# Kernel optimization log

Measured on AMD Instinct MI355X. Metric: run time of the kernel, lower is better.

Reference implementation:

```python
import jax, jax.numpy as jnp
import numpy as np

DIM = 384
HEADS = 6
DIM_HEAD = 64
INNER = HEADS * DIM_HEAD  # 384


def setup_inputs() -> dict:
    key = jax.random.key(0)
    ks = jax.random.split(key, 6)
    s = 0.02
    return {
        "x_q": jax.random.normal(ks[0], (8, 4096, DIM), dtype=jnp.float32),
        "x_kv": jax.random.normal(ks[1], (8, 4096, DIM), dtype=jnp.float32),
        "Wq": jax.random.normal(ks[2], (DIM, INNER), dtype=jnp.float32) * s,
        "Wkv": jax.random.normal(ks[3], (DIM, 2 * INNER), dtype=jnp.float32) * s,
        "Wout": jax.random.normal(ks[4], (INNER, DIM), dtype=jnp.float32) * s,
        "bout": jax.random.normal(ks[5], (DIM,), dtype=jnp.float32) * s,
    }


def _split_heads(t, b, n):
    # [b, n, h*d] -> [b, h, n, d]
    return t.reshape(b, n, HEADS, DIM_HEAD).transpose(0, 2, 1, 3)


def reference(x_q, x_kv, Wq, Wkv, Wout, bout):
    b, nq, _ = x_q.shape
    nkv = x_kv.shape[1]
    q = x_q @ Wq                      # [b, nq, inner]
    kv_proj = x_kv @ Wkv              # [b, nkv, 2*inner]
    k, v = jnp.split(kv_proj, 2, axis=-1)
    q = _split_heads(q, b, nq)        # [b, h, nq, d]
    k = _split_heads(k, b, nkv)       # [b, h, nkv, d]
    v = _split_heads(v, b, nkv)       # [b, h, nkv, d]
    q = jax.nn.elu(q) + 1.0
    k = jax.nn.elu(k) + 1.0
    kv = jnp.einsum('bhnd,bhnm->bhdm', k, v)             # [b, h, d, d]
    z = 1.0 / (jnp.einsum('bhnd,bhd->bhn', q, k.sum(axis=2)) + 1e-6)
    out = jnp.einsum('bhnd,bhdm->bhnm', q, kv) * z[..., None]  # [b, h, nq, d]
    out = out.transpose(0, 2, 1, 3).reshape(b, nq, INNER)
    return out @ Wout + bout
```

## Files before the change

kernel.cpp:

```cpp
#include <hip/hip_runtime.h>
#include <math.h>

#define BATCH 8
#define SEQ 4096
#define DIMSZ 384
#define HEADS 6
#define DH 64
#define MTOT (BATCH * SEQ)
#define KD 384

typedef short short8 __attribute__((ext_vector_type(8)));
typedef float floatx4 __attribute__((ext_vector_type(4)));
typedef unsigned short ushort4v __attribute__((ext_vector_type(4)));
typedef unsigned short ushort8v __attribute__((ext_vector_type(8)));
typedef unsigned int uint2v __attribute__((ext_vector_type(2)));
typedef unsigned int uint4v __attribute__((ext_vector_type(4)));

__device__ __forceinline__ float elu1(float x) { return x > 0.f ? x + 1.f : __expf(x); }

__device__ __forceinline__ unsigned short f2b(float f) {
    unsigned int u = __float_as_uint(f);
    u = (u + 0x7fffu + ((u >> 16) & 1u)) >> 16;
    return (unsigned short)u;
}
__device__ __forceinline__ float b2f(unsigned short u) {
    return __uint_as_float(((unsigned int)u) << 16);
}
__device__ __forceinline__ unsigned int f2b2(float lo, float hi) {
    unsigned int r;
    asm("v_cvt_pk_bf16_f32 %0, %1, %2" : "=v"(r) : "v"(lo), "v"(hi));
    return r;
}

__device__ __forceinline__ void gl16(const void* g, void* l) {
    __builtin_amdgcn_global_load_lds((const __attribute__((address_space(1))) unsigned int*)g,
                                     (__attribute__((address_space(3))) unsigned int*)l, 16, 0, 0);
}

#define BARRIER_EXEMPT8()                                              \
    do {                                                               \
        asm volatile("s_waitcnt vmcnt(8) lgkmcnt(0)" ::: "memory");    \
        __builtin_amdgcn_s_barrier();                                  \
        __builtin_amdgcn_sched_barrier(0);                             \
    } while (0)
#define BARRIER_EXEMPT4()                                              \
    do {                                                               \
        asm volatile("s_waitcnt vmcnt(4) lgkmcnt(0)" ::: "memory");    \
        __builtin_amdgcn_s_barrier();                                  \
        __builtin_amdgcn_sched_barrier(0);                             \
    } while (0)
#define BARRIER_DRAIN()                                                \
    do {                                                               \
        asm volatile("s_waitcnt vmcnt(0) lgkmcnt(0)" ::: "memory");    \
        __builtin_amdgcn_s_barrier();                                  \
        __builtin_amdgcn_sched_barrier(0);                             \
    } while (0)

__global__ __launch_bounds__(256) void conv_wt3(const float* __restrict__ Wq,
                                                const float* __restrict__ Wkv,
                                                const float* __restrict__ Wout,
                                                unsigned short* __restrict__ WqT,
                                                unsigned short* __restrict__ WkvT,
                                                unsigned short* __restrict__ WoutT) {
    __shared__ float tile[32][33];
    int bx = blockIdx.x;
    const float* W;
    unsigned short* WT;
    int N;
    if (bx < 12) { W = Wq; WT = WqT; N = DIMSZ; }
    else if (bx < 36) { W = Wkv; WT = WkvT; N = 2 * DIMSZ; bx -= 12; }
    else { W = Wout; WT = WoutT; N = DIMSZ; bx -= 36; }
    const int n0 = bx * 32, k0 = blockIdx.y * 32;
    const int tx = threadIdx.x & 31, ty = threadIdx.x >> 5;
#pragma unroll
    for (int i = 0; i < 32; i += 8) tile[ty + i][tx] = W[(size_t)(k0 + ty + i) * N + n0 + tx];
    __syncthreads();
#pragma unroll
    for (int i = 0; i < 32; i += 8)
        WT[(size_t)(n0 + ty + i) * KD + k0 + tx] = f2b(tile[tx][ty + i]);
}

__global__ __launch_bounds__(256, 3) void gemm_kv(const float* __restrict__ A,
                                                  const unsigned short* __restrict__ WkvT,
                                                  float* __restrict__ pkv,
                                                  float* __restrict__ pks) {
    __shared__ __align__(16) unsigned short buf[17408];
    __shared__ float ksLDS[128];
    unsigned short* As = buf;
    unsigned short* Bs = buf + 8192;
    const int tid = threadIdx.x;
    const int lane = tid & 63, wave = tid >> 6;
    const int l15 = lane & 15, qd = lane >> 4;
    const int fid = blockIdx.x;
    const int xcd = fid & 7;
    const int s = fid >> 3;
    const int h = s % HEADS;
    const int rtl = s / HEADS;
    const int row0 = (xcd * 32 + rtl) * 128;
    const int pidx = (xcd * HEADS + h) * 32 + rtl;
    const int wm = (wave & 1) * 64, wn = (wave >> 1) * 64;

    const float* Ab = A + (size_t)row0 * KD;
    const unsigned short* Bb = WkvT + (size_t)(h * DH) * KD;
    const int srow = tid >> 3;
    const int scol = (((tid & 7) ^ (srow & 7)) * 8);

    floatx4 zero = {0.f, 0.f, 0.f, 0.f};
    floatx4 acc[4][4];
#pragma unroll
    for (int i = 0; i < 4; ++i)
#pragma unroll
        for (int j = 0; j < 4; ++j) acc[i][j] = zero;

    const int sw = l15 & 7;
    float4 g0[4], g1[4];
#pragma unroll
    for (int i = 0; i < 4; ++i) {
        const float* src = Ab + (size_t)(i * 32 + srow) * KD + scol;
        g0[i] = *(const float4*)src;
        g1[i] = *(const float4*)(src + 4);
    }
#pragma unroll
    for (int kk = 0; kk < KD; kk += 64) {
        __syncthreads();
#pragma unroll
        for (int i = 0; i < 4; ++i)
            gl16(Bb + (size_t)(i * 32 + srow + (i >= 2 ? 320 : 0)) * KD + kk + scol,
                 Bs + i * 2048 + wave * 512);
#pragma unroll
        for (int i = 0; i < 4; ++i) {
            uint4v u;
            u[0] = f2b2(g0[i].x, g0[i].y);
            u[1] = f2b2(g0[i].z, g0[i].w);
            u[2] = f2b2(g1[i].x, g1[i].y);
            u[3] = f2b2(g1[i].z, g1[i].w);
            *(uint4v*)&As[i * 2048 + tid * 8] = u;
        }
        if (kk + 64 < KD) {
#pragma unroll
            for (int i = 0; i < 4; ++i) {
                const float* src = Ab + (size_t)(i * 32 + srow) * KD + kk + 64 + scol;
                g0[i] = *(const float4*)src;
                g1[i] = *(const float4*)(src + 4);
            }
            BARRIER_EXEMPT8();
        } else {
            BARRIER_DRAIN();
        }
#pragma unroll
        for (int t = 0; t < 2; ++t) {
            const int chnk = ((t * 4 + qd) ^ sw) * 8;
            short8 af[4], bfr[4];
#pragma unroll
            for (int mi = 0; mi < 4; ++mi)
                af[mi] = *(const short8*)&As[(wm + mi * 16 + l15) * 64 + chnk];
#pragma unroll
            for (int ni = 0; ni < 4; ++ni)
                bfr[ni] = *(const short8*)&Bs[(wn + ni * 16 + l15) * 64 + chnk];
#pragma unroll
            for (int mi = 0; mi < 4; ++mi)
#pragma unroll
                for (int ni = 0; ni < 4; ++ni)
                    acc[mi][ni] = __builtin_amdgcn_mfma_f32_16x16x32_bf16(af[mi], bfr[ni],
                                                                          acc[mi][ni], 0, 0, 0);
        }
    }

    __syncthreads();
    const bool kw = (wn == 0);
    float ksp[4] = {};
#pragma unroll
    for (int mi = 0; mi < 4; ++mi)
#pragma unroll
        for (int ni = 0; ni < 4; ++ni) {
            const int rb = wm + mi * 16 + qd * 4;
            const int cl = wn + ni * 16 + l15;
            float v0 = acc[mi][ni][0], v1 = acc[mi][ni][1];
            float v2 = acc[mi][ni][2], v3 = acc[mi][ni][3];
            if (kw) {
                v0 = elu1(v0); v1 = elu1(v1); v2 = elu1(v2); v3 = elu1(v3);
                ksp[ni] += (v0 + v1) + (v2 + v3);
            }
            uint2v o;
            o[0] = f2b2(v0, v1);
            o[1] = f2b2(v2, v3);
            *(uint2v*)&buf[cl * 136 + rb] = o;
        }
    if (kw) {
#pragma unroll
        for (int ni = 0; ni < 4; ++ni) {
            float v = ksp[ni];
            v += __shfl_xor(v, 16);
            v += __shfl_xor(v, 32);
            if (lane < 16) ksLDS[wave * 64 + ni * 16 + lane] = v;
        }
    }
    __syncthreads();
    floatx4 kva[4];
#pragma unroll
    for (int j = 0; j < 4; ++j) kva[j] = zero;
#pragma unroll
    for (int nk = 0; nk < 4; ++nk) {
        short8 afk = *(const short8*)&buf[(wave * 16 + l15) * 136 + nk * 32 + qd * 8];
#pragma unroll
        for (int nj = 0; nj < 4; ++nj) {
            short8 bfv = *(const short8*)&buf[(64 + nj * 16 + l15) * 136 + nk * 32 + qd * 8];
            kva[nj] = __builtin_amdgcn_mfma_f32_16x16x32_bf16(afk, bfv, kva[nj], 0, 0, 0);
        }
    }
    float* P = pkv + (size_t)pidx * 4096;
#pragma unroll
    for (int nj = 0; nj < 4; ++nj)
#pragma unroll
        for (int r = 0; r < 4; ++r)
            P[(wave * 16 + qd * 4 + r) * 64 + nj * 16 + l15] = kva[nj][r];
    if (tid < 64) pks[pidx * 64 + tid] = ksLDS[tid] + ksLDS[64 + tid];
}

__global__ __launch_bounds__(256) void kv_reduce(const float* __restrict__ pkv,
                                                 const float* __restrict__ pks,
                                                 unsigned short* __restrict__ kv_bf,
                                                 float* __restrict__ ksum_g) {
    const int bh = blockIdx.x >> 2, dc = blockIdx.x & 3;
    const int tid = threadIdx.x;
    unsigned short* kb = kv_bf + (size_t)bh * 4096;
    const int i0 = dc * 1024 + tid * 4;
    float4 sum = {0.f, 0.f, 0.f, 0.f};
#pragma unroll
    for (int c = 0; c < 32; ++c) {
        float4 p = *(const float4*)&pkv[(size_t)(bh * 32 + c) * 4096 + i0];
        sum.x += p.x; sum.y += p.y; sum.z += p.z; sum.w += p.w;
    }
    const int d = i0 >> 6, m = i0 & 63;
    kb[(m + 0) * 64 + d] = f2b(sum.x);
    kb[(m + 1) * 64 + d] = f2b(sum.y);
    kb[(m + 2) * 64 + d] = f2b(sum.z);
    kb[(m + 3) * 64 + d] = f2b(sum.w);
    if (dc == 0 && tid < 64) {
        float s = 0.f;
#pragma unroll
        for (int c = 0; c < 32; ++c) s += pks[(bh * 32 + c) * 64 + tid];
        ksum_g[bh * 64 + tid] = s;
    }
}

__global__ __launch_bounds__(256, 3) void gemm_q_attn(const float* __restrict__ A,
                                                      const unsigned short* __restrict__ WqT,
                                                      const unsigned short* __restrict__ kv_bf,
                                                      const float* __restrict__ ksum_g,
                                                      unsigned short* __restrict__ attn) {
    __shared__ __align__(16) unsigned short buf[17408];
    __shared__ float ksh[128];
    __shared__ float zsh[256];
    unsigned short* As = buf;
    unsigned short* Bs = buf + 8192;
    const int tid = threadIdx.x;
    const int lane = tid & 63, wave = tid >> 6;
    const int l15 = lane & 15, qd = lane >> 4;
    const int fid = blockIdx.x;
    const int xcd = fid & 7;
    const int s = fid >> 3;
    const int ct = s % 3;
    const int rtl = s / 3;
    const int row0 = (xcd * 32 + rtl) * 128;
    const int col0 = ct * 128;
    const int bh0 = xcd * HEADS + ct * 2;
    const int wd = (wave & 1) * 64, wn2 = (wave >> 1) * 64;

    if (tid < 128) ksh[tid] = ksum_g[bh0 * 64 + tid];

    const float* Ab = A + (size_t)row0 * KD;
    const unsigned short* Bb = WqT + (size_t)col0 * KD;
    const int srow = tid >> 3;
    const int scol = (((tid & 7) ^ (srow & 7)) * 8);

    floatx4 zero = {0.f, 0.f, 0.f, 0.f};
    floatx4 acc[4][4];
#pragma unroll
    for (int i = 0; i < 4; ++i)
#pragma unroll
        for (int j = 0; j < 4; ++j) acc[i][j] = zero;

    const int sw = l15 & 7;
    float4 g0[4], g1[4];
#pragma unroll
    for (int i = 0; i < 4; ++i) {
        const float* src = Ab + (size_t)(i * 32 + srow) * KD + scol;
        g0[i] = *(const float4*)src;
        g1[i] = *(const float4*)(src + 4);
    }
#pragma unroll
    for (int kk = 0; kk < KD; kk += 64) {
        __syncthreads();
#pragma unroll
        for (int i = 0; i < 4; ++i)
            gl16(Bb + (size_t)(i * 32 + srow) * KD + kk + scol, Bs + i * 2048 + wave * 512);
#pragma unroll
        for (int i = 0; i < 4; ++i) {
            uint4v u;
            u[0] = f2b2(g0[i].x, g0[i].y);
            u[1] = f2b2(g0[i].z, g0[i].w);
            u[2] = f2b2(g1[i].x, g1[i].y);
            u[3] = f2b2(g1[i].z, g1[i].w);
            *(uint4v*)&As[i * 2048 + tid * 8] = u;
        }
        if (kk + 64 < KD) {
#pragma unroll
            for (int i = 0; i < 4; ++i) {
                const float* src = Ab + (size_t)(i * 32 + srow) * KD + kk + 64 + scol;
                g0[i] = *(const float4*)src;
                g1[i] = *(const float4*)(src + 4);
            }
            BARRIER_EXEMPT8();
        } else {
            BARRIER_DRAIN();
        }
#pragma unroll
        for (int t = 0; t < 2; ++t) {
            const int chnk = ((t * 4 + qd) ^ sw) * 8;
            short8 wf[4], xf[4];
#pragma unroll
            for (int di = 0; di < 4; ++di)
                wf[di] = *(const short8*)&Bs[(wd + di * 16 + l15) * 64 + chnk];
#pragma unroll
            for (int nj = 0; nj < 4; ++nj)
                xf[nj] = *(const short8*)&As[(wn2 + nj * 16 + l15) * 64 + chnk];
#pragma unroll
            for (int di = 0; di < 4; ++di)
#pragma unroll
                for (int nj = 0; nj < 4; ++nj)
                    acc[di][nj] = __builtin_amdgcn_mfma_f32_16x16x32_bf16(wf[di], xf[nj],
                                                                          acc[di][nj], 0, 0, 0);
        }
    }

    float zp[4] = {};
#pragma unroll
    for (int di = 0; di < 4; ++di)
#pragma unroll
        for (int r = 0; r < 4; ++r) {
            const float ks = ksh[wd + di * 16 + qd * 4 + r];
#pragma unroll
            for (int nj = 0; nj < 4; ++nj) {
                const float q = elu1(acc[di][nj][r]);
                acc[di][nj][r] = q;
                zp[nj] += q * ks;
            }
        }
#pragma unroll
    for (int nj = 0; nj < 4; ++nj) {
        float v = zp[nj];
        v += __shfl_xor(v, 16);
        v += __shfl_xor(v, 32);
        zp[nj] = 1.f / (v + 1e-6f);
    }
    __syncthreads();
    if (lane < 16) {
#pragma unroll
        for (int nj = 0; nj < 4; ++nj) zsh[(wave & 1) * 128 + wn2 + nj * 16 + lane] = zp[nj];
    }
#pragma unroll
    for (int di = 0; di < 4; ++di)
#pragma unroll
        for (int nj = 0; nj < 4; ++nj) {
            const int rb = wd + di * 16 + qd * 4;
            const int cl = wn2 + nj * 16 + l15;
            uint2v o;
            o[0] = f2b2(acc[di][nj][0], acc[di][nj][1]);
            o[1] = f2b2(acc[di][nj][2], acc[di][nj][3]);
            *(uint2v*)&buf[cl * 136 + rb] = o;
        }
    __syncthreads();
    const int hh = wave & 1;
    const unsigned short* kvB = kv_bf + (size_t)(bh0 + hh) * 4096;
    floatx4 acc2[4][4];
#pragma unroll
    for (int i = 0; i < 4; ++i)
#pragma unroll
        for (int j = 0; j < 4; ++j) acc2[i][j] = zero;
#pragma unroll
    for (int t = 0; t < 2; ++t) {
        short8 bf2[4];
#pragma unroll
        for (int bj = 0; bj < 4; ++bj)
            bf2[bj] = *(const short8*)&kvB[(bj * 16 + l15) * 64 + t * 32 + qd * 8];
#pragma unroll
        for (int ai = 0; ai < 4; ++ai) {
            short8 af =
                *(const short8*)&buf[(wn2 + ai * 16 + l15) * 136 + hh * 64 + t * 32 + qd * 8];
#pragma unroll
            for (int bj = 0; bj < 4; ++bj)
                acc2[ai][bj] =
                    __builtin_amdgcn_mfma_f32_16x16x32_bf16(af, bf2[bj], acc2[ai][bj], 0, 0, 0);
        }
    }
#pragma unroll
    for (int ai = 0; ai < 4; ++ai)
#pragma unroll
        for (int bj = 0; bj < 4; ++bj) {
            const int colg = col0 + hh * 64 + bj * 16 + l15;
#pragma unroll
            for (int r = 0; r < 4; ++r) {
                const int nl = wn2 + ai * 16 + qd * 4 + r;
                const float v = acc2[ai][bj][r] * zsh[hh * 128 + nl];
                attn[(size_t)(row0 + nl) * KD + colg] = f2b(v);
            }
        }
}

__global__ __launch_bounds__(256, 4) void gemm_out(const unsigned short* __restrict__ A,
                                                   const unsigned short* __restrict__ BT,
                                                   float* __restrict__ C,
                                                   const float* __restrict__ bias) {
    __shared__ __align__(16) unsigned short buf[17408];
    unsigned short* As = buf;
    unsigned short* Bs = buf + 8192;
    const int tid = threadIdx.x;
    const int lane = tid & 63, wave = tid >> 6;
    const int l15 = lane & 15, qd = lane >> 4;
    const int fid = blockIdx.x;
    const int xcd = fid & 7;
    const int s = fid >> 3;
    const int row0 = (xcd * 32 + s / 3) * 128;
    const int col0 = (s % 3) * 128;
    const int wm = (wave & 1) * 64, wn = (wave >> 1) * 64;

    const unsigned short* Ab = A + (size_t)row0 * KD;
    const unsigned short* Bb = BT + (size_t)col0 * KD;
    const int srow = tid >> 3;
    const int scol = (((tid & 7) ^ (srow & 7)) * 8);

    floatx4 zero = {0.f, 0.f, 0.f, 0.f};
    floatx4 acc[4][4];
#pragma unroll
    for (int i = 0; i < 4; ++i)
#pragma unroll
        for (int j = 0; j < 4; ++j) acc[i][j] = zero;

    const int sw = l15 & 7;
    ushort8v ga[4];
#pragma unroll
    for (int i = 0; i < 4; ++i)
        ga[i] = *(const ushort8v*)(Ab + (size_t)(i * 32 + srow) * KD + scol);
#pragma unroll
    for (int kk = 0; kk < KD; kk += 64) {
        __syncthreads();
#pragma unroll
        for (int i = 0; i < 4; ++i)
            gl16(Bb + (size_t)(i * 32 + srow) * KD + kk + scol, Bs + i * 2048 + wave * 512);
#pragma unroll
        for (int i = 0; i < 4; ++i)
            *(ushort8v*)&As[i * 2048 + tid * 8] = ga[i];
        if (kk + 64 < KD) {
#pragma unroll
            for (int i = 0; i < 4; ++i)
                ga[i] = *(const ushort8v*)(Ab + (size_t)(i * 32 + srow) * KD + kk + 64 + scol);
            BARRIER_EXEMPT4();
        } else {
            BARRIER_DRAIN();
        }
#pragma unroll
        for (int t = 0; t < 2; ++t) {
            const int chnk = ((t * 4 + qd) ^ sw) * 8;
            short8 af[4], bfr[4];
#pragma unroll
            for (int mi = 0; mi < 4; ++mi)
                af[mi] = *(const short8*)&As[(wm + mi * 16 + l15) * 64 + chnk];
#pragma unroll
            for (int ni = 0; ni < 4; ++ni)
                bfr[ni] = *(const short8*)&Bs[(wn + ni * 16 + l15) * 64 + chnk];
#pragma unroll
            for (int mi = 0; mi < 4; ++mi)
#pragma unroll
                for (int ni = 0; ni < 4; ++ni)
                    acc[mi][ni] = __builtin_amdgcn_mfma_f32_16x16x32_bf16(af[mi], bfr[ni],
                                                                          acc[mi][ni], 0, 0, 0);
        }
    }
#pragma unroll
    for (int mi = 0; mi < 4; ++mi)
#pragma unroll
        for (int ni = 0; ni < 4; ++ni) {
            const int rbase = row0 + wm + mi * 16 + qd * 4;
            const int col = col0 + wn + ni * 16 + l15;
            const float bsv = bias[col];
#pragma unroll
            for (int r = 0; r < 4; ++r)
                __builtin_nontemporal_store(acc[mi][ni][r] + bsv,
                                            &C[(size_t)(rbase + r) * DIMSZ + col]);
        }
}

extern "C" void kernel_launch(void* const* d_in, const int* in_sizes, int n_in,
                              void* d_out, int out_size, void* d_ws, size_t ws_size,
                              hipStream_t stream) {
    const float* x_q = (const float*)d_in[0];
    const float* x_kv = (const float*)d_in[1];
    const float* Wq = (const float*)d_in[2];
    const float* Wkv = (const float*)d_in[3];
    const float* Wout = (const float*)d_in[4];
    const float* bout = (const float*)d_in[5];
    float* out = (float*)d_out;

    char* ws = (char*)d_ws;
    float* pkv = (float*)(ws + 0);
    unsigned short* attn_bf = (unsigned short*)(ws + 0);
    unsigned short* WqT = (unsigned short*)(ws + 25165824);
    unsigned short* WkvT = (unsigned short*)(ws + 25460736);
    unsigned short* WoutT = (unsigned short*)(ws + 26050560);
    float* ksum = (float*)(ws + 26345472);
    float* pks = (float*)(ws + 26357760);
    unsigned short* kv_bf = (unsigned short*)(ws + 26750976);

    dim3 blk(256);
    conv_wt3<<<dim3(48, 12), blk, 0, stream>>>(Wq, Wkv, Wout, WqT, WkvT, WoutT);
    gemm_kv<<<dim3(1536), blk, 0, stream>>>(x_kv, WkvT, pkv, pks);
    kv_reduce<<<dim3(192), blk, 0, stream>>>(pkv, pks, kv_bf, ksum);
    gemm_q_attn<<<dim3(768), blk, 0, stream>>>(x_q, WqT, kv_bf, ksum, attn_bf);
    gemm_out<<<dim3(768), blk, 0, stream>>>(attn_bf, WoutT, out, bout);
}
```

Baseline: 227.9 us.

## Double-buffer B tiles in LDS and restructure GEMM main loops

The three GEMM kernels now double-buffer the weight (B) tile in LDS. The next B slice is fetched via global_load_lds into the alternate buffer while MFMA runs on the current one, and the A tile is written to LDS after the compute, between two barriers. The goal is to hide global load latency behind matrix math and drop the partial vmcnt waits at the top of each iteration. LDS per block grows, and gemm_out's launch bound drops from 4 to 3 blocks per CU, so occupancy falls.

```diff
diff --git a/kernel.cpp b/kernel.cpp
--- a/kernel.cpp
+++ b/kernel.cpp
@@ -11,7 +11,6 @@
 
 typedef short short8 __attribute__((ext_vector_type(8)));
 typedef float floatx4 __attribute__((ext_vector_type(4)));
-typedef unsigned short ushort4v __attribute__((ext_vector_type(4)));
 typedef unsigned short ushort8v __attribute__((ext_vector_type(8)));
 typedef unsigned int uint2v __attribute__((ext_vector_type(2)));
 typedef unsigned int uint4v __attribute__((ext_vector_type(4)));
@@ -23,9 +22,6 @@
     u = (u + 0x7fffu + ((u >> 16) & 1u)) >> 16;
     return (unsigned short)u;
 }
-__device__ __forceinline__ float b2f(unsigned short u) {
-    return __uint_as_float(((unsigned int)u) << 16);
-}
 __device__ __forceinline__ unsigned int f2b2(float lo, float hi) {
     unsigned int r;
     asm("v_cvt_pk_bf16_f32 %0, %1, %2" : "=v"(r) : "v"(lo), "v"(hi));
@@ -37,23 +33,18 @@
                                      (__attribute__((address_space(3))) unsigned int*)l, 16, 0, 0);
 }
 
-#define BARRIER_EXEMPT8()                                              \
-    do {                                                               \
-        asm volatile("s_waitcnt vmcnt(8) lgkmcnt(0)" ::: "memory");    \
-        __builtin_amdgcn_s_barrier();                                  \
-        __builtin_amdgcn_sched_barrier(0);                             \
+#define SB0() __builtin_amdgcn_sched_barrier(0)
+#define BAR_SOFT()                     \
+    do {                               \
+        SB0();                         \
+        __builtin_amdgcn_s_barrier();  \
+        SB0();                         \
     } while (0)
-#define BARRIER_EXEMPT4()                                              \
-    do {                                                               \
-        asm volatile("s_waitcnt vmcnt(4) lgkmcnt(0)" ::: "memory");    \
-        __builtin_amdgcn_s_barrier();                                  \
-        __builtin_amdgcn_sched_barrier(0);                             \
-    } while (0)
-#define BARRIER_DRAIN()                                                \
-    do {                                                               \
-        asm volatile("s_waitcnt vmcnt(0) lgkmcnt(0)" ::: "memory");    \
-        __builtin_amdgcn_s_barrier();                                  \
-        __builtin_amdgcn_sched_barrier(0);                             \
+#define BAR_STAGE()                                                 \
+    do {                                                            \
+        asm volatile("s_waitcnt vmcnt(0) lgkmcnt(0)" ::: "memory"); \
+        __builtin_amdgcn_s_barrier();                               \
+        SB0();                                                      \
     } while (0)
 
 __global__ __launch_bounds__(256) void conv_wt3(const float* __restrict__ Wq,
@@ -84,10 +75,11 @@
                                                   const unsigned short* __restrict__ WkvT,
                                                   float* __restrict__ pkv,
                                                   float* __restrict__ pks) {
-    __shared__ __align__(16) unsigned short buf[17408];
+    __shared__ __align__(16) unsigned short buf[24576];
     __shared__ float ksLDS[128];
     unsigned short* As = buf;
-    unsigned short* Bs = buf + 8192;
+    unsigned short* Bs0 = buf + 8192;
+    unsigned short* Bs1 = buf + 16384;
     const int tid = threadIdx.x;
     const int lane = tid & 63, wave = tid >> 6;
     const int l15 = lane & 15, qd = lane >> 4;
@@ -115,54 +107,73 @@
     const int sw = l15 & 7;
     float4 g0[4], g1[4];
 #pragma unroll
+    for (int i = 0; i < 4; ++i)
+        gl16(Bb + (size_t)(i * 32 + srow + (i >= 2 ? 320 : 0)) * KD + scol,
+             Bs0 + i * 2048 + wave * 512);
+#pragma unroll
     for (int i = 0; i < 4; ++i) {
         const float* src = Ab + (size_t)(i * 32 + srow) * KD + scol;
         g0[i] = *(const float4*)src;
         g1[i] = *(const float4*)(src + 4);
     }
 #pragma unroll
-    for (int kk = 0; kk < KD; kk += 64) {
-        __syncthreads();
-#pragma unroll
-        for (int i = 0; i < 4; ++i)
-            gl16(Bb + (size_t)(i * 32 + srow + (i >= 2 ? 320 : 0)) * KD + kk + scol,
-                 Bs + i * 2048 + wave * 512);
-#pragma unroll
-        for (int i = 0; i < 4; ++i) {
-            uint4v u;
-            u[0] = f2b2(g0[i].x, g0[i].y);
-            u[1] = f2b2(g0[i].z, g0[i].w);
-            u[2] = f2b2(g1[i].x, g1[i].y);
-            u[3] = f2b2(g1[i].z, g1[i].w);
-            *(uint4v*)&As[i * 2048 + tid * 8] = u;
-        }
-        if (kk + 64 < KD) {
+    for (int i = 0; i < 4; ++i) {
+        uint4v u;
+        u[0] = f2b2(g0[i].x, g0[i].y);
+        u[1] = f2b2(g0[i].z, g0[i].w);
+        u[2] = f2b2(g1[i].x, g1[i].y);
+        u[3] = f2b2(g1[i].z, g1[i].w);
+        *(uint4v*)&As[i * 2048 + tid * 8] = u;
+    }
+    BAR_STAGE();
+
+#pragma unroll
+    for (int t = 0; t < 6; ++t) {
+        unsigned short* Bc = (t & 1) ? Bs1 : Bs0;
+        if (t < 5) {
+            unsigned short* Bn = (t & 1) ? Bs0 : Bs1;
+            const int kn = t * 64 + 64;
+#pragma unroll
+            for (int i = 0; i < 4; ++i)
+                gl16(Bb + (size_t)(i * 32 + srow + (i >= 2 ? 320 : 0)) * KD + kn + scol,
+                     Bn + i * 2048 + wave * 512);
 #pragma unroll
             for (int i = 0; i < 4; ++i) {
-                const float* src = Ab + (size_t)(i * 32 + srow) * KD + kk + 64 + scol;
+                const float* src = Ab + (size_t)(i * 32 + srow) * KD + kn + scol;
                 g0[i] = *(const float4*)src;
                 g1[i] = *(const float4*)(src + 4);
             }
-            BARRIER_EXEMPT8();
-        } else {
-            BARRIER_DRAIN();
-        }
-#pragma unroll
-        for (int t = 0; t < 2; ++t) {
-            const int chnk = ((t * 4 + qd) ^ sw) * 8;
+            SB0();
+        }
+#pragma unroll
+        for (int tt = 0; tt < 2; ++tt) {
+            const int chnk = ((tt * 4 + qd) ^ sw) * 8;
             short8 af[4], bfr[4];
 #pragma unroll
             for (int mi = 0; mi < 4; ++mi)
                 af[mi] = *(const short8*)&As[(wm + mi * 16 + l15) * 64 + chnk];
 #pragma unroll
             for (int ni = 0; ni < 4; ++ni)
-                bfr[ni] = *(const short8*)&Bs[(wn + ni * 16 + l15) * 64 + chnk];
+                bfr[ni] = *(const short8*)&Bc[(wn + ni * 16 + l15) * 64 + chnk];
 #pragma unroll
             for (int mi = 0; mi < 4; ++mi)
 #pragma unroll
                 for (int ni = 0; ni < 4; ++ni)
                     acc[mi][ni] = __builtin_amdgcn_mfma_f32_16x16x32_bf16(af[mi], bfr[ni],
                                                                           acc[mi][ni], 0, 0, 0);
+        }
+        if (t < 5) {
+            BAR_SOFT();
+#pragma unroll
+            for (int i = 0; i < 4; ++i) {
+                uint4v u;
+                u[0] = f2b2(g0[i].x, g0[i].y);
+                u[1] = f2b2(g0[i].z, g0[i].w);
+                u[2] = f2b2(g1[i].x, g1[i].y);
+                u[3] = f2b2(g1[i].z, g1[i].w);
+                *(uint4v*)&As[i * 2048 + tid * 8] = u;
+            }
+            BAR_STAGE();
         }
     }
 
@@ -249,11 +260,12 @@
                                                       const unsigned short* __restrict__ kv_bf,
                                                       const float* __restrict__ ksum_g,
                                                       unsigned short* __restrict__ attn) {
-    __shared__ __align__(16) unsigned short buf[17408];
+    __shared__ __align__(16) unsigned short buf[24576];
     __shared__ float ksh[128];
     __shared__ float zsh[256];
     unsigned short* As = buf;
-    unsigned short* Bs = buf + 8192;
+    unsigned short* Bs0 = buf + 8192;
+    unsigned short* Bs1 = buf + 16384;
     const int tid = threadIdx.x;
     const int lane = tid & 63, wave = tid >> 6;
     const int l15 = lane & 15, qd = lane >> 4;
@@ -284,44 +296,49 @@
     const int sw = l15 & 7;
     float4 g0[4], g1[4];
 #pragma unroll
+    for (int i = 0; i < 4; ++i)
+        gl16(Bb + (size_t)(i * 32 + srow) * KD + scol, Bs0 + i * 2048 + wave * 512);
+#pragma unroll
     for (int i = 0; i < 4; ++i) {
         const float* src = Ab + (size_t)(i * 32 + srow) * KD + scol;
         g0[i] = *(const float4*)src;
         g1[i] = *(const float4*)(src + 4);
     }
 #pragma unroll
-    for (int kk = 0; kk < KD; kk += 64) {
-        __syncthreads();
-#pragma unroll
-        for (int i = 0; i < 4; ++i)
-            gl16(Bb + (size_t)(i * 32 + srow) * KD + kk + scol, Bs + i * 2048 + wave * 512);
-#pragma unroll
-        for (int i = 0; i < 4; ++i) {
-            uint4v u;
-            u[0] = f2b2(g0[i].x, g0[i].y);
-            u[1] = f2b2(g0[i].z, g0[i].w);
-            u[2] = f2b2(g1[i].x, g1[i].y);
-            u[3] = f2b2(g1[i].z, g1[i].w);
-            *(uint4v*)&As[i * 2048 + tid * 8] = u;
-        }
-        if (kk + 64 < KD) {
+    for (int i = 0; i < 4; ++i) {
+        uint4v u;
+        u[0] = f2b2(g0[i].x, g0[i].y);
+        u[1] = f2b2(g0[i].z, g0[i].w);
+        u[2] = f2b2(g1[i].x, g1[i].y);
+        u[3] = f2b2(g1[i].z, g1[i].w);
+        *(uint4v*)&As[i * 2048 + tid * 8] = u;
+    }
+    BAR_STAGE();
+
+#pragma unroll
+    for (int t = 0; t < 6; ++t) {
+        unsigned short* Bc = (t & 1) ? Bs1 : Bs0;
+        if (t < 5) {
+            unsigned short* Bn = (t & 1) ? Bs0 : Bs1;
+            const int kn = t * 64 + 64;
+#pragma unroll
+            for (int i = 0; i < 4; ++i)
+                gl16(Bb + (size_t)(i * 32 + srow) * KD + kn + scol, Bn + i * 2048 + wave * 512);
 #pragma unroll
             for (int i = 0; i < 4; ++i) {
-                const float* src = Ab + (size_t)(i * 32 + srow) * KD + kk + 64 + scol;
+                const float* src = Ab + (size_t)(i * 32 + srow) * KD + kn + scol;
                 g0[i] = *(const float4*)src;
                 g1[i] = *(const float4*)(src + 4);
             }
-            BARRIER_EXEMPT8();
-        } else {
-            BARRIER_DRAIN();
-        }
-#pragma unroll
-        for (int t = 0; t < 2; ++t) {
-            const int chnk = ((t * 4 + qd) ^ sw) * 8;
+            SB0();
+        }
+#pragma unroll
+        for (int tt = 0; tt < 2; ++tt) {
+            const int chnk = ((tt * 4 + qd) ^ sw) * 8;
             short8 wf[4], xf[4];
 #pragma unroll
             for (int di = 0; di < 4; ++di)
-                wf[di] = *(const short8*)&Bs[(wd + di * 16 + l15) * 64 + chnk];
+                wf[di] = *(const short8*)&Bc[(wd + di * 16 + l15) * 64 + chnk];
 #pragma unroll
             for (int nj = 0; nj < 4; ++nj)
                 xf[nj] = *(const short8*)&As[(wn2 + nj * 16 + l15) * 64 + chnk];
@@ -331,6 +348,19 @@
                 for (int nj = 0; nj < 4; ++nj)
                     acc[di][nj] = __builtin_amdgcn_mfma_f32_16x16x32_bf16(wf[di], xf[nj],
                                                                           acc[di][nj], 0, 0, 0);
+        }
+        if (t < 5) {
+            BAR_SOFT();
+#pragma unroll
+            for (int i = 0; i < 4; ++i) {
+                uint4v u;
+                u[0] = f2b2(g0[i].x, g0[i].y);
+                u[1] = f2b2(g0[i].z, g0[i].w);
+                u[2] = f2b2(g1[i].x, g1[i].y);
+                u[3] = f2b2(g1[i].z, g1[i].w);
+                *(uint4v*)&As[i * 2048 + tid * 8] = u;
+            }
+            BAR_STAGE();
         }
     }
 
@@ -408,13 +438,14 @@
         }
 }
 
-__global__ __launch_bounds__(256, 4) void gemm_out(const unsigned short* __restrict__ A,
+__global__ __launch_bounds__(256, 3) void gemm_out(const unsigned short* __restrict__ A,
                                                    const unsigned short* __restrict__ BT,
                                                    float* __restrict__ C,
                                                    const float* __restrict__ bias) {
-    __shared__ __align__(16) unsigned short buf[17408];
+    __shared__ __align__(16) unsigned short buf[24576];
     unsigned short* As = buf;
-    unsigned short* Bs = buf + 8192;
+    unsigned short* Bs0 = buf + 8192;
+    unsigned short* Bs1 = buf + 16384;
     const int tid = threadIdx.x;
     const int lane = tid & 63, wave = tid >> 6;
     const int l15 = lane & 15, qd = lane >> 4;
@@ -441,40 +472,50 @@
     ushort8v ga[4];
 #pragma unroll
     for (int i = 0; i < 4; ++i)
+        gl16(Bb + (size_t)(i * 32 + srow) * KD + scol, Bs0 + i * 2048 + wave * 512);
+#pragma unroll
+    for (int i = 0; i < 4; ++i)
         ga[i] = *(const ushort8v*)(Ab + (size_t)(i * 32 + srow) * KD + scol);
 #pragma unroll
-    for (int kk = 0; kk < KD; kk += 64) {
-        __syncthreads();
-#pragma unroll
-        for (int i = 0; i < 4; ++i)
-            gl16(Bb + (size_t)(i * 32 + srow) * KD + kk + scol, Bs + i * 2048 + wave * 512);
-#pragma unroll
-        for (int i = 0; i < 4; ++i)
-            *(ushort8v*)&As[i * 2048 + tid * 8] = ga[i];
-        if (kk + 64 < KD) {
+    for (int i = 0; i < 4; ++i) *(ushort8v*)&As[i * 2048 + tid * 8] = ga[i];
+    BAR_STAGE();
+
+#pragma unroll
+    for (int t = 0; t < 6; ++t) {
+        unsigned short* Bc = (t & 1) ? Bs1 : Bs0;
+        if (t < 5) {
+            unsigned short* Bn = (t & 1) ? Bs0 : Bs1;
+            const int kn = t * 64 + 64;
 #pragma unroll
             for (int i = 0; i < 4; ++i)
-                ga[i] = *(const ushort8v*)(Ab + (size_t)(i * 32 + srow) * KD + kk + 64 + scol);
-            BARRIER_EXEMPT4();
-        } else {
-            BARRIER_DRAIN();
-        }
-#pragma unroll
-        for (int t = 0; t < 2; ++t) {
-            const int chnk = ((t * 4 + qd) ^ sw) * 8;
+                gl16(Bb + (size_t)(i * 32 + srow) * KD + kn + scol, Bn + i * 2048 + wave * 512);
+#pragma unroll
+            for (int i = 0; i < 4; ++i)
+                ga[i] = *(const ushort8v*)(Ab + (size_t)(i * 32 + srow) * KD + kn + scol);
+            SB0();
+        }
+#pragma unroll
+        for (int tt = 0; tt < 2; ++tt) {
+            const int chnk = ((tt * 4 + qd) ^ sw) * 8;
             short8 af[4], bfr[4];
 #pragma unroll
             for (int mi = 0; mi < 4; ++mi)
                 af[mi] = *(const short8*)&As[(wm + mi * 16 + l15) * 64 + chnk];
 #pragma unroll
             for (int ni = 0; ni < 4; ++ni)
-                bfr[ni] = *(const short8*)&Bs[(wn + ni * 16 + l15) * 64 + chnk];
+                bfr[ni] = *(const short8*)&Bc[(wn + ni * 16 + l15) * 64 + chnk];
 #pragma unroll
             for (int mi = 0; mi < 4; ++mi)
 #pragma unroll
                 for (int ni = 0; ni < 4; ++ni)
                     acc[mi][ni] = __builtin_amdgcn_mfma_f32_16x16x32_bf16(af[mi], bfr[ni],
                                                                           acc[mi][ni], 0, 0, 0);
+        }
+        if (t < 5) {
+            BAR_SOFT();
+#pragma unroll
+            for (int i = 0; i < 4; ++i) *(ushort8v*)&As[i * 2048 + tid * 8] = ga[i];
+            BAR_STAGE();
         }
     }
 #pragma unroll
```

After: 216.2 us, median of 2. -5.1%, faster.
